# Performance work log

Hardware: AMD Instinct MI355X
Metric: run time of the kernel (lower is better)

Reference implementation:

```python
import jax, jax.numpy as jnp
import numpy as np

F = 26          # number of sparse fields
V = 100000      # vocab per field
D = 32          # embedding dim
DENSE = 13
HID = (1024, 512, 256)
B = 16384


def setup_inputs() -> dict:
    key = jax.random.key(0)
    ks = jax.random.split(key, 16)
    x_sparse = jax.random.randint(ks[0], (B, F), 0, V, dtype=jnp.int32)
    x_dense = jax.random.normal(ks[1], (B, DENSE), dtype=jnp.float32)
    emb_tables = jax.random.normal(ks[2], (F, V, D), dtype=jnp.float32) * 0.05
    lin_tables = jax.random.normal(ks[3], (F, V), dtype=jnp.float32) * 0.05
    dnn_in = F * D + DENSE
    dims = (dnn_in,) + HID
    params = {}
    for i in range(len(HID)):
        params[f'W{i}'] = jax.random.normal(ks[4 + i], (dims[i], dims[i + 1]), dtype=jnp.float32) * (1.0 / np.sqrt(dims[i]))
        params[f'b{i}'] = jnp.zeros((dims[i + 1],), dtype=jnp.float32)
    Wout = jax.random.normal(ks[10], (HID[-1], 1), dtype=jnp.float32) * (1.0 / np.sqrt(HID[-1]))
    bout = jnp.zeros((1,), dtype=jnp.float32)
    return dict(x_sparse=x_sparse, x_dense=x_dense, emb_tables=emb_tables,
                lin_tables=lin_tables,
                W0=params['W0'], b0=params['b0'],
                W1=params['W1'], b1=params['b1'],
                W2=params['W2'], b2=params['b2'],
                Wout=Wout, bout=bout)


def reference(x_sparse, x_dense, emb_tables, lin_tables,
              W0, b0, W1, b1, W2, b2, Wout, bout):
    f_idx = jnp.arange(F)[None, :]            # [1, F]
    # batched multi-field gather: [B, F, D] and [B, F]
    emb = emb_tables[f_idx, x_sparse]          # [B, F, D]
    lin = lin_tables[f_idx, x_sparse]          # [B, F]
    linear_logit = lin.sum(axis=1)             # [B]
    # FM pairwise sum_{i<j} <e_i, e_j> via sum-square identity
    s = emb.sum(axis=1)                        # [B, D]
    fm_logit = 0.5 * ((s * s).sum(axis=-1) - (emb * emb).sum(axis=(1, 2)))  # [B]
    # DNN on concatenated embeddings + dense feats
    h = jnp.concatenate([emb.reshape(emb.shape[0], F * D), x_dense], axis=1)
    h = jax.nn.relu(h @ W0 + b0)
    h = jax.nn.relu(h @ W1 + b1)
    h = jax.nn.relu(h @ W2 + b2)
    dnn_logit = (h @ Wout + bout)[:, 0]        # [B]
    return jax.nn.sigmoid(linear_logit + fm_logit + dnn_logit)
```

## Files before the change

### kernel.cpp

```cpp
#include <hip/hip_runtime.h>
#include <math.h>


typedef __attribute__((ext_vector_type(8))) short shortx8;
typedef __attribute__((ext_vector_type(4))) float floatx4;

#define AS1 __attribute__((address_space(1)))
#define AS3 __attribute__((address_space(3)))

__device__ __forceinline__ void load_lds_16(const void* g, void* l) {
    __builtin_amdgcn_global_load_lds((AS1 void*)g, (AS3 void*)l, 16, 0, 0);
}

__device__ __forceinline__ unsigned short f2bf(float x) {
    union { float f; unsigned int u; } v; v.f = x;
    unsigned int r = v.u + 0x7fffu + ((v.u >> 16) & 1u);
    return (unsigned short)(r >> 16);
}

__device__ __forceinline__
void wtrans_tile(const float* __restrict__ W, unsigned short* __restrict__ Wt,
                 int K, int N, int Kpad, int bx, int by, int tid)
{
    __shared__ float tile[32][33];
    const int k0 = bx * 32, n0 = by * 32;
    const int tx = tid & 31, ty = tid >> 5;
#pragma unroll
    for (int i = 0; i < 32; i += 8) {
        int k = k0 + ty + i;
        tile[ty + i][tx] = (k < K) ? W[(size_t)k * N + (n0 + tx)] : 0.f;
    }
    __syncthreads();
#pragma unroll
    for (int i = 0; i < 32; i += 8) {
        int n = n0 + ty + i, kk = k0 + tx;
        Wt[(size_t)n * Kpad + kk] = f2bf(tile[tx][ty + i]);
    }
}

__global__ __launch_bounds__(256)
void prep(const int* __restrict__ xs, const float* __restrict__ xd,
          const float* __restrict__ emb, const float* __restrict__ lint,
          const float* __restrict__ W0, const float* __restrict__ W1,
          const float* __restrict__ W2,
          unsigned short* __restrict__ h0, float* __restrict__ lg,
          unsigned short* __restrict__ Wt0, unsigned short* __restrict__ Wt1,
          unsigned short* __restrict__ Wt2)
{
    const int bid = blockIdx.x;
    const int tid = threadIdx.x;

    if (bid >= 4096) {
        int t = bid - 4096;
        if (t < 896)       wtrans_tile(W0, Wt0, 845, 1024, 896, t % 28, t / 28, tid);
        else if (t < 1408) wtrans_tile(W1, Wt1, 1024, 512, 1024, (t - 896) % 32, (t - 896) / 32, tid);
        else               wtrans_tile(W2, Wt2, 512, 256, 512, (t - 1408) % 16, (t - 1408) / 16, tid);
        return;
    }

    const int lane = tid & 63;
    const int wave = tid >> 6;
    const int b = bid * 4 + wave;

    int idx = 0; float linv = 0.f;
    if (lane < 26) {
        idx = xs[b * 26 + lane];
        linv = lint[(size_t)lane * 100000 + idx];
    }
    const int d = lane & 31;
    const int half = lane >> 5;
    float s = 0.f, sq = 0.f;
    unsigned short* hrow = h0 + (size_t)b * 896;
#pragma unroll
    for (int it = 0; it < 13; ++it) {
        int f = it * 2 + half;
        int fidx = __shfl(idx, f);
        float v = emb[((size_t)f * 100000 + (size_t)fidx) * 32 + d];
        s += v; sq += v * v;
        hrow[f * 32 + d] = f2bf(v);
    }
    s += __shfl_xor(s, 32);
    float t = 0.25f * s * s - 0.5f * sq + linv;
#pragma unroll
    for (int off = 32; off >= 1; off >>= 1) t += __shfl_xor(t, off);
    if (lane == 0) lg[b] = t;

    if (lane < 13) hrow[832 + lane] = f2bf(xd[b * 13 + lane]);
    else           hrow[832 + lane] = 0;
}

__global__ __launch_bounds__(256, 2)
void gemm_bign(const unsigned short* __restrict__ X,
               const unsigned short* __restrict__ Wt,
               const float* __restrict__ bias,
               unsigned short* __restrict__ Y,
               int M, int N, int K)
{
    __shared__ alignas(16) unsigned short As[128 * 64];
    __shared__ alignas(16) unsigned short Bs[256 * 64];

    const int tid  = threadIdx.x;
    const int lane = tid & 63;
    const int wave = tid >> 6;
    const int bm = blockIdx.x * 128;
    const int bn = blockIdx.y * 256;
    const int wm = (wave & 1) * 64;
    const int wn = (wave >> 1) * 128;
    const int lrow  = lane & 15;
    const int lquad = lane >> 4;

    floatx4 acc[4][8];
    const floatx4 z4 = {0.f, 0.f, 0.f, 0.f};
#pragma unroll
    for (int i = 0; i < 4; ++i)
#pragma unroll
        for (int j = 0; j < 8; ++j) acc[i][j] = z4;

    for (int k0 = 0; k0 < K; k0 += 64) {
#pragma unroll
        for (int q = 0; q < 4; ++q) {
            int c = tid + q * 256;
            load_lds_16(X + (size_t)(bm + (c >> 3)) * K + (k0 + (c & 7) * 8),
                        As + (size_t)c * 8);
        }
#pragma unroll
        for (int q = 0; q < 8; ++q) {
            int c = tid + q * 256;
            load_lds_16(Wt + (size_t)(bn + (c >> 3)) * K + (k0 + (c & 7) * 8),
                        Bs + (size_t)c * 8);
        }
        __syncthreads();

#pragma unroll
        for (int s = 0; s < 2; ++s) {
            shortx8 a[4];
#pragma unroll
            for (int i = 0; i < 4; ++i)
                a[i] = *(const shortx8*)(As + (wm + i * 16 + lrow) * 64 + s * 32 + lquad * 8);
#pragma unroll
            for (int j = 0; j < 8; ++j) {
                shortx8 b = *(const shortx8*)(Bs + (wn + j * 16 + lrow) * 64 + s * 32 + lquad * 8);
#pragma unroll
                for (int i = 0; i < 4; ++i)
                    acc[i][j] = __builtin_amdgcn_mfma_f32_16x16x32_bf16(a[i], b, acc[i][j], 0, 0, 0);
            }
        }
        __syncthreads();
    }

#pragma unroll
    for (int i = 0; i < 4; ++i) {
        const int row = bm + wm + i * 16 + lquad * 4;
#pragma unroll
        for (int j = 0; j < 8; ++j) {
            const int col = bn + wn + j * 16 + lrow;
            const float bv = bias[col];
#pragma unroll
            for (int r = 0; r < 4; ++r) {
                float v = fmaxf(acc[i][j][r] + bv, 0.f);
                Y[(size_t)(row + r) * N + col] = f2bf(v);
            }
        }
    }
}

__global__ __launch_bounds__(256)
void gemm3_final(const unsigned short* __restrict__ X,
                 const unsigned short* __restrict__ Wt,
                 const float* __restrict__ bias,
                 const float* __restrict__ Wo,
                 const float* __restrict__ bo,
                 const float* __restrict__ lg,
                 float* __restrict__ out)
{
    const int K = 512;
    __shared__ alignas(16) unsigned short As[64 * 32];
    __shared__ alignas(16) unsigned short Bs[256 * 32];
    __shared__ float red[4][64];

    const int tid  = threadIdx.x;
    const int lane = tid & 63;
    const int wave = tid >> 6;
    const int bm = blockIdx.x * 64;
    const int wn = wave * 64;
    const int lrow  = lane & 15;
    const int lquad = lane >> 4;

    floatx4 acc[4][4];
    const floatx4 z4 = {0.f, 0.f, 0.f, 0.f};
#pragma unroll
    for (int i = 0; i < 4; ++i)
#pragma unroll
        for (int j = 0; j < 4; ++j) acc[i][j] = z4;

    const int ar = tid >> 2, akp = (tid & 3) << 3;

    for (int k0 = 0; k0 < K; k0 += 32) {
        load_lds_16(X + (size_t)(bm + ar) * K + (k0 + akp), As + (size_t)tid * 8);
#pragma unroll
        for (int q = 0; q < 4; ++q) {
            int c = tid + q * 256;
            load_lds_16(Wt + (size_t)(c >> 2) * K + (k0 + akp), Bs + (size_t)c * 8);
        }
        __syncthreads();

        shortx8 a[4], b[4];
#pragma unroll
        for (int i = 0; i < 4; ++i)
            a[i] = *(const shortx8*)(As + (i * 16 + lrow) * 32 + lquad * 8);
#pragma unroll
        for (int j = 0; j < 4; ++j)
            b[j] = *(const shortx8*)(Bs + (wn + j * 16 + lrow) * 32 + lquad * 8);
#pragma unroll
        for (int i = 0; i < 4; ++i)
#pragma unroll
            for (int j = 0; j < 4; ++j)
                acc[i][j] = __builtin_amdgcn_mfma_f32_16x16x32_bf16(a[i], b[j], acc[i][j], 0, 0, 0);
        __syncthreads();
    }

    float bv[4], wv[4];
#pragma unroll
    for (int j = 0; j < 4; ++j) {
        int col = wn + j * 16 + lrow;
        bv[j] = bias[col];
        wv[j] = Wo[col];
    }
#pragma unroll
    for (int i = 0; i < 4; ++i) {
#pragma unroll
        for (int r = 0; r < 4; ++r) {
            float p = 0.f;
#pragma unroll
            for (int j = 0; j < 4; ++j) {
                float v = fmaxf(acc[i][j][r] + bv[j], 0.f);
                p += v * wv[j];
            }
            p += __shfl_xor(p, 1);
            p += __shfl_xor(p, 2);
            p += __shfl_xor(p, 4);
            p += __shfl_xor(p, 8);
            if (lrow == 0) red[wave][i * 16 + lquad * 4 + r] = p;
        }
    }
    __syncthreads();
    if (tid < 64) {
        float s = red[0][tid] + red[1][tid] + red[2][tid] + red[3][tid];
        float x = s + bo[0] + lg[bm + tid];
        out[bm + tid] = 1.f / (1.f + expf(-x));
    }
}

extern "C" void kernel_launch(void* const* d_in, const int* in_sizes, int n_in,
                              void* d_out, int out_size, void* d_ws, size_t ws_size,
                              hipStream_t stream)
{
    const int*   xs = (const int*)d_in[0];
    const float* xd = (const float*)d_in[1];
    const float* em = (const float*)d_in[2];
    const float* li = (const float*)d_in[3];
    const float* W0 = (const float*)d_in[4];
    const float* b0 = (const float*)d_in[5];
    const float* W1 = (const float*)d_in[6];
    const float* b1 = (const float*)d_in[7];
    const float* W2 = (const float*)d_in[8];
    const float* b2 = (const float*)d_in[9];
    const float* Wo = (const float*)d_in[10];
    const float* bo = (const float*)d_in[11];
    float* out = (float*)d_out;

    char* ws = (char*)d_ws;
    unsigned short* h0  = (unsigned short*)(ws);
    unsigned short* h1  = (unsigned short*)(ws + 29360128);
    unsigned short* h2  = (unsigned short*)(ws);
    unsigned short* Wt0 = (unsigned short*)(ws + 62914560);
    unsigned short* Wt1 = (unsigned short*)(ws + 64749568);
    unsigned short* Wt2 = (unsigned short*)(ws + 65798144);
    float*          lg  = (float*)(ws + 66060288);

    prep<<<5632, 256, 0, stream>>>(xs, xd, em, li, W0, W1, W2, h0, lg, Wt0, Wt1, Wt2);

    gemm_bign<<<dim3(128, 4), 256, 0, stream>>>(h0, Wt0, b0, h1, 16384, 1024, 896);
    gemm_bign<<<dim3(128, 2), 256, 0, stream>>>(h1, Wt1, b1, h2, 16384, 512, 1024);
    gemm3_final<<<256, 256, 0, stream>>>(h2, Wt2, b2, Wo, bo, lg, out);
}
```

Before: 493.6 us.

## Replace GEMM kernels with 4-stage pipelined, swizzled, 512-thread MFMA GEMM

Replaces the single-buffered GEMM with a templated kernel that prefetches K-slices of 32 into a 4-deep LDS ring using async global-to-LDS loads and explicit vmcnt waits. This overlaps memory with MFMA work instead of stalling on a barrier every iteration. It also XOR-swizzles the LDS layout to avoid bank conflicts and remaps block IDs for L2 locality. Layer-0 tiles grow to 256x256 with 8 waves. The cost is more registers and LDS, which may limit occupancy, plus finer-grained barriers.

Measured after the change: 498.1 us. No clear change (+0.9%).

```diff
diff --git a/kernel.cpp b/kernel.cpp
--- a/kernel.cpp
+++ b/kernel.cpp
@@ -16,6 +16,17 @@
     union { float f; unsigned int u; } v; v.f = x;
     unsigned int r = v.u + 0x7fffu + ((v.u >> 16) & 1u);
     return (unsigned short)(r >> 16);
+}
+
+template<int N>
+__device__ __forceinline__ void waitvm() {
+    asm volatile("s_waitcnt vmcnt(%0)" :: "n"(N) : "memory");
+}
+
+__device__ __forceinline__ void bar() {
+    asm volatile("" ::: "memory");
+    __builtin_amdgcn_s_barrier();
+    asm volatile("" ::: "memory");
 }
 
 __device__ __forceinline__
@@ -89,70 +100,102 @@
     else           hrow[832 + lane] = 0;
 }
 
-__global__ __launch_bounds__(256, 2)
-void gemm_bign(const unsigned short* __restrict__ X,
+template<int BM, int BN>
+__global__ __launch_bounds__(512, 2)
+void gemm_pipe(const unsigned short* __restrict__ X,
                const unsigned short* __restrict__ Wt,
                const float* __restrict__ bias,
                unsigned short* __restrict__ Y,
-               int M, int N, int K)
-{
-    __shared__ alignas(16) unsigned short As[128 * 64];
-    __shared__ alignas(16) unsigned short Bs[256 * 64];
-
-    const int tid  = threadIdx.x;
-    const int lane = tid & 63;
-    const int wave = tid >> 6;
-    const int bm = blockIdx.x * 128;
-    const int bn = blockIdx.y * 256;
-    const int wm = (wave & 1) * 64;
-    const int wn = (wave >> 1) * 128;
+               int M, int N, int K, int nby)
+{
+    constexpr int CA  = BM / 128;
+    constexpr int CB  = BN / 128;
+    constexpr int LPT = CA + CB;
+    constexpr int MR  = BM / 32;
+    constexpr int NR  = BN / 64;
+
+    __shared__ alignas(16) unsigned short As[4][BM * 32];
+    __shared__ alignas(16) unsigned short Bs[4][BN * 32];
+
+    const int tid   = threadIdx.x;
+    const int lane  = tid & 63;
+    const int wave  = tid >> 6;
     const int lrow  = lane & 15;
     const int lquad = lane >> 4;
-
-    floatx4 acc[4][8];
+    const int wm = (wave >> 2) * (BM / 2);
+    const int wn = (wave & 3) * (BN / 4);
+
+    const int nwg = gridDim.x;
+    const int bid = blockIdx.x;
+    const int swz = (bid & 7) * (nwg >> 3) + (bid >> 3);
+    const int bx = swz / nby, by = swz % nby;
+    const int bm = bx * BM, bn = by * BN;
+
+    floatx4 acc[MR][NR];
     const floatx4 z4 = {0.f, 0.f, 0.f, 0.f};
 #pragma unroll
-    for (int i = 0; i < 4; ++i)
-#pragma unroll
-        for (int j = 0; j < 8; ++j) acc[i][j] = z4;
-
-    for (int k0 = 0; k0 < K; k0 += 64) {
-#pragma unroll
-        for (int q = 0; q < 4; ++q) {
-            int c = tid + q * 256;
-            load_lds_16(X + (size_t)(bm + (c >> 3)) * K + (k0 + (c & 7) * 8),
-                        As + (size_t)c * 8);
-        }
-#pragma unroll
-        for (int q = 0; q < 8; ++q) {
-            int c = tid + q * 256;
-            load_lds_16(Wt + (size_t)(bn + (c >> 3)) * K + (k0 + (c & 7) * 8),
-                        Bs + (size_t)c * 8);
-        }
-        __syncthreads();
-
-#pragma unroll
-        for (int s = 0; s < 2; ++s) {
-            shortx8 a[4];
-#pragma unroll
-            for (int i = 0; i < 4; ++i)
-                a[i] = *(const shortx8*)(As + (wm + i * 16 + lrow) * 64 + s * 32 + lquad * 8);
-#pragma unroll
-            for (int j = 0; j < 8; ++j) {
-                shortx8 b = *(const shortx8*)(Bs + (wn + j * 16 + lrow) * 64 + s * 32 + lquad * 8);
-#pragma unroll
-                for (int i = 0; i < 4; ++i)
-                    acc[i][j] = __builtin_amdgcn_mfma_f32_16x16x32_bf16(a[i], b, acc[i][j], 0, 0, 0);
-            }
-        }
-        __syncthreads();
-    }
-
-#pragma unroll
-    for (int i = 0; i < 4; ++i) {
+    for (int i = 0; i < MR; ++i)
+#pragma unroll
+        for (int j = 0; j < NR; ++j) acc[i][j] = z4;
+
+    const int NT = K >> 5;
+
+    auto STAGE = [&](int tt) {
+        const int k0 = tt << 5;
+        unsigned short* a_dst = As[tt & 3];
+        unsigned short* b_dst = Bs[tt & 3];
+#pragma unroll
+        for (int q = 0; q < CA; ++q) {
+            int c = tid + q * 512;
+            int row = c >> 2, sl = c & 3;
+            load_lds_16(X + (size_t)(bm + row) * K + (k0 + ((sl ^ (row & 3)) << 3)),
+                        a_dst + c * 8);
+        }
+#pragma unroll
+        for (int q = 0; q < CB; ++q) {
+            int c = tid + q * 512;
+            int row = c >> 2, sl = c & 3;
+            load_lds_16(Wt + (size_t)(bn + row) * K + (k0 + ((sl ^ (row & 3)) << 3)),
+                        b_dst + c * 8);
+        }
+    };
+
+    STAGE(0); STAGE(1); STAGE(2);
+
+    const int abase = (wm + lrow) * 32 + ((lquad ^ (lrow & 3)) << 3);
+    const int bbase = (wn + lrow) * 32 + ((lquad ^ (lrow & 3)) << 3);
+
+    for (int t = 0; t < NT; ++t) {
+        const int cur = t & 3;
+        if (t + 3 < NT)      { STAGE(t + 3); waitvm<3 * LPT>(); }
+        else if (t + 2 < NT) waitvm<2 * LPT>();
+        else if (t + 1 < NT) waitvm<LPT>();
+        else                 waitvm<0>();
+        bar();
+
+        shortx8 a[MR], b[NR];
+#pragma unroll
+        for (int i = 0; i < MR; ++i)
+            a[i] = *(const shortx8*)(&As[cur][abase + i * 512]);
+#pragma unroll
+        for (int j = 0; j < NR; ++j)
+            b[j] = *(const shortx8*)(&Bs[cur][bbase + j * 512]);
+
+        __builtin_amdgcn_s_setprio(1);
+#pragma unroll
+        for (int i = 0; i < MR; ++i)
+#pragma unroll
+            for (int j = 0; j < NR; ++j)
+                acc[i][j] = __builtin_amdgcn_mfma_f32_16x16x32_bf16(a[i], b[j], acc[i][j], 0, 0, 0);
+        __builtin_amdgcn_s_setprio(0);
+        bar();
+    }
+
+#pragma unroll
+    for (int i = 0; i < MR; ++i) {
         const int row = bm + wm + i * 16 + lquad * 4;
 #pragma unroll
-        for (int j = 0; j < 8; ++j) {
+        for (int j = 0; j < NR; ++j) {
             const int col = bn + wn + j * 16 + lrow;
             const float bv = bias[col];
 #pragma unroll
@@ -280,7 +323,7 @@
 
     prep<<<5632, 256, 0, stream>>>(xs, xd, em, li, W0, W1, W2, h0, lg, Wt0, Wt1, Wt2);
 
-    gemm_bign<<<dim3(128, 4), 256, 0, stream>>>(h0, Wt0, b0, h1, 16384, 1024, 896);
-    gemm_bign<<<dim3(128, 2), 256, 0, stream>>>(h1, Wt1, b1, h2, 16384, 512, 1024);
+    gemm_pipe<256, 256><<<256, 512, 0, stream>>>(h0, Wt0, b0, h1, 16384, 1024, 896, 4);
+    gemm_pipe<128, 256><<<256, 512, 0, stream>>>(h1, Wt1, b1, h2, 16384, 512, 1024, 2);
     gemm3_final<<<256, 256, 0, stream>>>(h2, Wt2, b2, Wo, bo, lg, out);
 }
```
